# Performance work log

Hardware: AMD Instinct MI355X
Metric: run time of the kernel (lower is better)

The kernel has to match this reference:

```python
import jax, jax.numpy as jnp
import numpy as np

B, D, H = 2048, 64, 512  # batch, state dim, vf hidden dim
IS_DIFFUSION = True      # vf output divided by 2.0 as in CNF.forward


def setup_inputs() -> dict:
    key = jax.random.key(0)
    ks = jax.random.split(key, 8)

    def lin(k, fi, fo):
        return jax.random.normal(k, (fi, fo), jnp.float32) / np.float32(np.sqrt(fi))

    return {
        "t": jax.random.uniform(ks[0], (1,), jnp.float32),      # scalar time, kept as [1]
        "x": jax.random.normal(ks[1], (B, D + 1), jnp.float32),  # last col = logp channel
        "W1": lin(ks[2], D + 1, H),
        "b1": jax.random.normal(ks[3], (H,), jnp.float32) * 0.01,
        "W2": lin(ks[4], H, H),
        "b2": jax.random.normal(ks[5], (H,), jnp.float32) * 0.01,
        "W3": lin(ks[6], H, D),
        "b3": jax.random.normal(ks[7], (D,), jnp.float32) * 0.01,
    }


def reference(t, x, W1, b1, W2, b2, W3, b3):
    scale = 2.0 if IS_DIFFUSION else 1.0
    xd = x[..., :-1]  # [B, D] -- drop augmented log-density channel

    def vf_single(xi):  # R^D -> R^D vector field, t and params closed over
        h = jnp.concatenate([xi, t])           # [D+1] (time-conditioned input)
        h = jnp.tanh(h @ W1 + b1)
        h = jnp.tanh(h @ W2 + b2)
        return (h @ W3 + b3) / scale

    dx = jax.vmap(vf_single)(xd)  # [B, D]
    # exact divergence: trace of per-sample Jacobian via reverse-mode (matches torch jacrev)
    div = jax.vmap(lambda xi: jnp.trace(jax.jacrev(vf_single)(xi)))(xd)  # [B]
    return jnp.concatenate([dx, div[:, None]], axis=-1)  # [B, D+1]
```

## Files before the change

### kernel.cpp

```cpp
#include <hip/hip_runtime.h>


constexpr int HD = 512;
constexpr int DD = 64;
constexpr int SB = 8;
constexpr int NB = 2048 / SB;

typedef __attribute__((ext_vector_type(8))) short bf16x8;
typedef __attribute__((ext_vector_type(4))) float f32x4;

__device__ inline unsigned short f2bf(float f) {
    union { float f; unsigned u; } v; v.f = f;
    return (unsigned short)((v.u + 0x7fffu + ((v.u >> 16) & 1u)) >> 16);
}
__device__ inline float fast_tanh(float xx) {
    float e = __expf(2.f * xx);
    return 1.f - 2.f / (e + 1.f);
}

__global__ __launch_bounds__(64) void cnf_pack_kernel(
    const float* __restrict__ W1, const float* __restrict__ W2,
    const float* __restrict__ W3, unsigned short* __restrict__ Bpack)
{
    __shared__ float w1s[64][33];
    __shared__ float w3s[16][65];
    const int b = blockIdx.x;
    const int mat = b >> 9, t = (b >> 4) & 31, kk = b & 15;
    const int l = threadIdx.x;
    const int q = l >> 4, nl = l & 15;
    const int n = t * 16 + nl;
    unsigned short o[8];
    if (mat == 0) {
#pragma unroll
        for (int j = 0; j < 8; ++j) {
            int k = kk * 32 + q * 8 + j;
            o[j] = f2bf(W2[k * HD + n]);
        }
    } else {
        for (int e = l; e < 64 * 32; e += 64) {
            int i = e >> 5, kl = e & 31;
            w1s[i][kl] = W1[i * HD + kk * 32 + kl];
        }
        for (int e = l; e < 16 * 64; e += 64) {
            int nn = e >> 6, i = e & 63;
            w3s[nn][i] = W3[(t * 16 + nn) * DD + i];
        }
        __syncthreads();
#pragma unroll
        for (int j = 0; j < 8; ++j) {
            int kl = q * 8 + j;
            float m = 0.f;
#pragma unroll 8
            for (int i = 0; i < 64; ++i) m += w1s[i][kl] * w3s[nl][i];
            o[j] = f2bf(W2[(kk * 32 + kl) * HD + n] * m);
        }
    }
    uint4 pk;
    pk.x = (unsigned)o[0] | ((unsigned)o[1] << 16);
    pk.y = (unsigned)o[2] | ((unsigned)o[3] << 16);
    pk.z = (unsigned)o[4] | ((unsigned)o[5] << 16);
    pk.w = (unsigned)o[6] | ((unsigned)o[7] << 16);
    const int w = t >> 2;
    const int t8 = mat * 4 + (t & 3);
    reinterpret_cast<uint4*>(Bpack)[((w * 16 + kk) * 8 + t8) * 64 + l] = pk;
}

__global__ __launch_bounds__(512, 2) void cnf_fused_kernel(
    const float* __restrict__ tptr, const float* __restrict__ x,
    const float* __restrict__ W1, const float* __restrict__ b1,
    const float* __restrict__ b2v, const float* __restrict__ W3,
    const float* __restrict__ b3, const unsigned short* __restrict__ Bpack,
    float* __restrict__ out)
{
    __shared__ float4 xsv[65 * 2];
    __shared__ unsigned short A_lds[16][520];
    __shared__ float4 h2v[HD * 2];
    __shared__ float4 divred[8][2];
    __shared__ float sm_b2[HD];

    const int tid  = threadIdx.x;
    const int s0   = blockIdx.x * SB;
    const int wave = tid >> 6, lane = tid & 63;

    const bf16x8* bp = reinterpret_cast<const bf16x8*>(Bpack)
                     + (size_t)wave * 8192 + lane;
    bf16x8 buf[3][8];
#pragma unroll
    for (int j = 0; j < 8; ++j) buf[0][j] = bp[j * 64];
#pragma unroll
    for (int j = 0; j < 8; ++j) buf[1][j] = bp[512 + j * 64];

    {
        const float tval = tptr[0];
        for (int e = tid; e < SB * 65; e += 512) {
            int s = e / 65, i = e % 65;
            reinterpret_cast<float*>(xsv)[i * SB + s] =
                (i == DD) ? tval : x[(s0 + s) * 65 + i];
        }
        sm_b2[tid] = b2v[tid];
    }
    __syncthreads();

    {
        const int u = tid;
        const float bb = b1[u];
        float2 a0 = {bb, bb}, a1 = {bb, bb}, a2 = {bb, bb}, a3 = {bb, bb};
        for (int ib = 0; ib < 64; ib += 16) {
            float w[16];
#pragma unroll
            for (int qq = 0; qq < 16; ++qq) w[qq] = W1[(ib + qq) * HD + u];
#pragma unroll
            for (int qq = 0; qq < 16; ++qq) {
                float4 p = xsv[2 * (ib + qq)], r = xsv[2 * (ib + qq) + 1];
                a0.x += p.x * w[qq]; a0.y += p.y * w[qq];
                a1.x += p.z * w[qq]; a1.y += p.w * w[qq];
                a2.x += r.x * w[qq]; a2.y += r.y * w[qq];
                a3.x += r.z * w[qq]; a3.y += r.w * w[qq];
            }
        }
        {
            float w = W1[64 * HD + u];
            float4 p = xsv[128], r = xsv[129];
            a0.x += p.x * w; a0.y += p.y * w;
            a1.x += p.z * w; a1.y += p.w * w;
            a2.x += r.x * w; a2.y += r.y * w;
            a3.x += r.z * w; a3.y += r.w * w;
        }
        float h[8] = {fast_tanh(a0.x), fast_tanh(a0.y), fast_tanh(a1.x), fast_tanh(a1.y),
                      fast_tanh(a2.x), fast_tanh(a2.y), fast_tanh(a3.x), fast_tanh(a3.y)};
#pragma unroll
        for (int s = 0; s < 8; ++s) {
            A_lds[s][u]     = f2bf(h[s]);
            A_lds[8 + s][u] = f2bf(1.f - h[s] * h[s]);
        }
    }
    __syncthreads();

    f32x4 cw[4], cg[4];
#pragma unroll
    for (int i = 0; i < 4; ++i) { cw[i] = (f32x4){0,0,0,0}; cg[i] = (f32x4){0,0,0,0}; }
    {
        const unsigned short* arow = &A_lds[lane & 15][0];
        const int aoff = (lane >> 4) * 8;
#pragma unroll
        for (int kk = 0; kk < 16; ++kk) {
            if (kk + 2 < 16) {
#pragma unroll
                for (int j = 0; j < 8; ++j)
                    buf[(kk + 2) % 3][j] = bp[(kk + 2) * 512 + j * 64];
            }
            bf16x8 af = *reinterpret_cast<const bf16x8*>(arow + kk * 32 + aoff);
#pragma unroll
            for (int i = 0; i < 4; ++i)
                cw[i] = __builtin_amdgcn_mfma_f32_16x16x32_bf16(af, buf[kk % 3][i], cw[i], 0, 0, 0);
#pragma unroll
            for (int i = 0; i < 4; ++i)
                cg[i] = __builtin_amdgcn_mfma_f32_16x16x32_bf16(af, buf[kk % 3][4 + i], cg[i], 0, 0, 0);
        }
    }

    {
        const int qd = lane >> 4;
        const int src = (lane >= 32) ? lane - 32 : lane;
        float4 dp = {0.f, 0.f, 0.f, 0.f};
#pragma unroll
        for (int i = 0; i < 4; ++i) {
            const int m = wave * 64 + i * 16 + (lane & 15);
            const float bb = sm_b2[m];
            float4 hv;
            hv.x = fast_tanh(cw[i][0] + bb);
            hv.y = fast_tanh(cw[i][1] + bb);
            hv.z = fast_tanh(cw[i][2] + bb);
            hv.w = fast_tanh(cw[i][3] + bb);
            if (lane < 32) h2v[2 * m + qd] = hv;
            float h0 = __shfl(hv.x, src), h1s = __shfl(hv.y, src);
            float h2s = __shfl(hv.z, src), h3s = __shfl(hv.w, src);
            dp.x += cg[i][0] * (1.f - h0 * h0);
            dp.y += cg[i][1] * (1.f - h1s * h1s);
            dp.z += cg[i][2] * (1.f - h2s * h2s);
            dp.w += cg[i][3] * (1.f - h3s * h3s);
        }
        if (lane >= 32) {
#pragma unroll
            for (int off = 8; off > 0; off >>= 1) {
                dp.x += __shfl_down(dp.x, off, 16);
                dp.y += __shfl_down(dp.y, off, 16);
                dp.z += __shfl_down(dp.z, off, 16);
                dp.w += __shfl_down(dp.w, off, 16);
            }
            if ((lane & 15) == 0) divred[wave][qd - 2] = dp;
        }
    }
    __syncthreads();

    float* opart = reinterpret_cast<float*>(A_lds);

    {
        const int k = lane, part = wave;
        float o[8];
#pragma unroll
        for (int q = 0; q < 8; ++q) o[q] = 0.f;
        const int mb = part * 64;
        for (int mm = 0; mm < 64; mm += 8) {
            float w[8];
#pragma unroll
            for (int q = 0; q < 8; ++q) w[q] = W3[(mb + mm + q) * DD + k];
#pragma unroll
            for (int q = 0; q < 8; ++q) {
                const int m = mb + mm + q;
                float4 ha = h2v[2 * m], hb = h2v[2 * m + 1];
                o[0] += ha.x * w[q]; o[1] += ha.y * w[q];
                o[2] += ha.z * w[q]; o[3] += ha.w * w[q];
                o[4] += hb.x * w[q]; o[5] += hb.y * w[q];
                o[6] += hb.z * w[q]; o[7] += hb.w * w[q];
            }
        }
#pragma unroll
        for (int q = 0; q < 8; ++q) opart[part * 512 + q * 64 + k] = o[q];
    }
    __syncthreads();

    {
        const int s = tid >> 6, k = tid & 63;
        float sum = b3[k];
#pragma unroll
        for (int p = 0; p < 8; ++p) sum += opart[p * 512 + s * 64 + k];
        out[(s0 + s) * 65 + k] = 0.5f * sum;
    }
    if (tid < 8) {
        const int qq = tid >> 2, r = tid & 3;
        float ds = 0.f;
#pragma unroll
        for (int w = 0; w < 8; ++w)
            ds += reinterpret_cast<const float*>(&divred[w][qq])[r];
        out[(s0 + tid) * 65 + DD] = 0.5f * ds;
    }
}

extern "C" void kernel_launch(void* const* d_in, const int* in_sizes, int n_in,
                              void* d_out, int out_size, void* d_ws, size_t ws_size,
                              hipStream_t stream) {
    const float* t  = (const float*)d_in[0];
    const float* x  = (const float*)d_in[1];
    const float* W1 = (const float*)d_in[2];
    const float* b1 = (const float*)d_in[3];
    const float* W2 = (const float*)d_in[4];
    const float* b2 = (const float*)d_in[5];
    const float* W3 = (const float*)d_in[6];
    const float* b3 = (const float*)d_in[7];
    float* out = (float*)d_out;
    unsigned short* Bpack = (unsigned short*)d_ws;

    cnf_pack_kernel<<<1024, 64, 0, stream>>>(W1, W2, W3, Bpack);
    cnf_fused_kernel<<<NB, 512, 0, stream>>>(t, x, W1, b1, b2, W3, b3, Bpack, out);
}
```

Measured before the change: 99.41 us.

## Merge weight packing into main kernel via cooperative launch and grid sync

Folds the separate bf16 weight-packing kernel into the fused kernel. Waves 0-3 of each block pack one slice of W2 or W2*(W1·W3), while waves 4-7 compute the first layer, and a grid-wide cooperative sync follows before the MFMA stage. This removes one kernel launch and overlaps packing with layer-1 compute. In exchange it adds a grid barrier, requires all 256 blocks to be co-resident, and raises shared memory use through a union buffer.

```diff
diff --git a/kernel.cpp b/kernel.cpp
--- a/kernel.cpp
+++ b/kernel.cpp
@@ -1,4 +1,7 @@
 #include <hip/hip_runtime.h>
+#include <hip/hip_cooperative_groups.h>
+
+namespace cg = cooperative_groups;
 
 
 constexpr int HD = 512;
@@ -18,77 +21,33 @@
     return 1.f - 2.f / (e + 1.f);
 }
 
-__global__ __launch_bounds__(64) void cnf_pack_kernel(
-    const float* __restrict__ W1, const float* __restrict__ W2,
-    const float* __restrict__ W3, unsigned short* __restrict__ Bpack)
-{
-    __shared__ float w1s[64][33];
-    __shared__ float w3s[16][65];
-    const int b = blockIdx.x;
-    const int mat = b >> 9, t = (b >> 4) & 31, kk = b & 15;
-    const int l = threadIdx.x;
-    const int q = l >> 4, nl = l & 15;
-    const int n = t * 16 + nl;
-    unsigned short o[8];
-    if (mat == 0) {
-#pragma unroll
-        for (int j = 0; j < 8; ++j) {
-            int k = kk * 32 + q * 8 + j;
-            o[j] = f2bf(W2[k * HD + n]);
-        }
-    } else {
-        for (int e = l; e < 64 * 32; e += 64) {
-            int i = e >> 5, kl = e & 31;
-            w1s[i][kl] = W1[i * HD + kk * 32 + kl];
-        }
-        for (int e = l; e < 16 * 64; e += 64) {
-            int nn = e >> 6, i = e & 63;
-            w3s[nn][i] = W3[(t * 16 + nn) * DD + i];
-        }
-        __syncthreads();
-#pragma unroll
-        for (int j = 0; j < 8; ++j) {
-            int kl = q * 8 + j;
-            float m = 0.f;
-#pragma unroll 8
-            for (int i = 0; i < 64; ++i) m += w1s[i][kl] * w3s[nl][i];
-            o[j] = f2bf(W2[(kk * 32 + kl) * HD + n] * m);
-        }
-    }
-    uint4 pk;
-    pk.x = (unsigned)o[0] | ((unsigned)o[1] << 16);
-    pk.y = (unsigned)o[2] | ((unsigned)o[3] << 16);
-    pk.z = (unsigned)o[4] | ((unsigned)o[5] << 16);
-    pk.w = (unsigned)o[6] | ((unsigned)o[7] << 16);
-    const int w = t >> 2;
-    const int t8 = mat * 4 + (t & 3);
-    reinterpret_cast<uint4*>(Bpack)[((w * 16 + kk) * 8 + t8) * 64 + l] = pk;
-}
-
-__global__ __launch_bounds__(512, 2) void cnf_fused_kernel(
+union SmemBig {
+    struct {
+        float w1s[64 * 132];
+        float w3s[16 * 65];
+    } pk;
+    float4 h2v[HD * 2];
+};
+
+__global__ __launch_bounds__(512, 2) void cnf_mega_kernel(
     const float* __restrict__ tptr, const float* __restrict__ x,
     const float* __restrict__ W1, const float* __restrict__ b1,
-    const float* __restrict__ b2v, const float* __restrict__ W3,
-    const float* __restrict__ b3, const unsigned short* __restrict__ Bpack,
-    float* __restrict__ out)
+    const float* __restrict__ W2, const float* __restrict__ b2v,
+    const float* __restrict__ W3, const float* __restrict__ b3,
+    unsigned short* __restrict__ Bpack, float* __restrict__ out)
 {
+    __shared__ SmemBig sm;
     __shared__ float4 xsv[65 * 2];
     __shared__ unsigned short A_lds[16][520];
-    __shared__ float4 h2v[HD * 2];
+    __shared__ float sm_b2[HD];
     __shared__ float4 divred[8][2];
-    __shared__ float sm_b2[HD];
 
     const int tid  = threadIdx.x;
-    const int s0   = blockIdx.x * SB;
+    const int blk  = blockIdx.x;
+    const int s0   = blk * SB;
     const int wave = tid >> 6, lane = tid & 63;
 
-    const bf16x8* bp = reinterpret_cast<const bf16x8*>(Bpack)
-                     + (size_t)wave * 8192 + lane;
-    bf16x8 buf[3][8];
-#pragma unroll
-    for (int j = 0; j < 8; ++j) buf[0][j] = bp[j * 64];
-#pragma unroll
-    for (int j = 0; j < 8; ++j) buf[1][j] = bp[512 + j * 64];
+    const int mat = blk & 1, t = (blk >> 1) & 31, kkg = blk >> 6;
 
     {
         const float tval = tptr[0];
@@ -98,50 +57,104 @@
                 (i == DD) ? tval : x[(s0 + s) * 65 + i];
         }
         sm_b2[tid] = b2v[tid];
-    }
-    __syncthreads();
-
-    {
-        const int u = tid;
-        const float bb = b1[u];
-        float2 a0 = {bb, bb}, a1 = {bb, bb}, a2 = {bb, bb}, a3 = {bb, bb};
-        for (int ib = 0; ib < 64; ib += 16) {
-            float w[16];
-#pragma unroll
-            for (int qq = 0; qq < 16; ++qq) w[qq] = W1[(ib + qq) * HD + u];
-#pragma unroll
-            for (int qq = 0; qq < 16; ++qq) {
-                float4 p = xsv[2 * (ib + qq)], r = xsv[2 * (ib + qq) + 1];
-                a0.x += p.x * w[qq]; a0.y += p.y * w[qq];
-                a1.x += p.z * w[qq]; a1.y += p.w * w[qq];
-                a2.x += r.x * w[qq]; a2.y += r.y * w[qq];
-                a3.x += r.z * w[qq]; a3.y += r.w * w[qq];
-            }
-        }
-        {
-            float w = W1[64 * HD + u];
-            float4 p = xsv[128], r = xsv[129];
-            a0.x += p.x * w; a0.y += p.y * w;
-            a1.x += p.z * w; a1.y += p.w * w;
-            a2.x += r.x * w; a2.y += r.y * w;
-            a3.x += r.z * w; a3.y += r.w * w;
-        }
-        float h[8] = {fast_tanh(a0.x), fast_tanh(a0.y), fast_tanh(a1.x), fast_tanh(a1.y),
-                      fast_tanh(a2.x), fast_tanh(a2.y), fast_tanh(a3.x), fast_tanh(a3.y)};
-#pragma unroll
-        for (int s = 0; s < 8; ++s) {
-            A_lds[s][u]     = f2bf(h[s]);
-            A_lds[8 + s][u] = f2bf(1.f - h[s] * h[s]);
-        }
-    }
-    __syncthreads();
-
-    f32x4 cw[4], cg[4];
-#pragma unroll
-    for (int i = 0; i < 4; ++i) { cw[i] = (f32x4){0,0,0,0}; cg[i] = (f32x4){0,0,0,0}; }
-    {
+        if (mat) {
+            for (int e = tid; e < 64 * 128; e += 512) {
+                int i = e >> 7, kl = e & 127;
+                sm.pk.w1s[i * 132 + kl] = W1[i * HD + kkg * 128 + kl];
+            }
+            for (int e = tid; e < 16 * 64; e += 512) {
+                int nn = e >> 6, i = e & 63;
+                sm.pk.w3s[nn * 65 + i] = W3[(t * 16 + nn) * DD + i];
+            }
+        }
+    }
+    __syncthreads();
+
+    if (wave < 4) {
+        const int kk = kkg * 4 + wave;
+        const int q = lane >> 4, nl = lane & 15;
+        const int n = t * 16 + nl;
+        unsigned short o[8];
+        if (mat == 0) {
+#pragma unroll
+            for (int j = 0; j < 8; ++j)
+                o[j] = f2bf(W2[(kk * 32 + q * 8 + j) * HD + n]);
+        } else {
+            float s[8];
+#pragma unroll
+            for (int j = 0; j < 8; ++j) s[j] = 0.f;
+            const int kl0 = wave * 32 + q * 8;
+#pragma unroll 4
+            for (int i = 0; i < 64; ++i) {
+                const float w3v = sm.pk.w3s[nl * 65 + i];
+#pragma unroll
+                for (int j = 0; j < 8; ++j)
+                    s[j] += sm.pk.w1s[i * 132 + kl0 + j] * w3v;
+            }
+#pragma unroll
+            for (int j = 0; j < 8; ++j)
+                o[j] = f2bf(W2[(kk * 32 + q * 8 + j) * HD + n] * s[j]);
+        }
+        uint4 pk4;
+        pk4.x = (unsigned)o[0] | ((unsigned)o[1] << 16);
+        pk4.y = (unsigned)o[2] | ((unsigned)o[3] << 16);
+        pk4.z = (unsigned)o[4] | ((unsigned)o[5] << 16);
+        pk4.w = (unsigned)o[6] | ((unsigned)o[7] << 16);
+        const int w = t >> 2, t8 = mat * 4 + (t & 3);
+        reinterpret_cast<uint4*>(Bpack)[((w * 16 + kk) * 8 + t8) * 64 + lane] = pk4;
+    } else {
+        const int u0 = tid - 256;
+#pragma unroll
+        for (int hu = 0; hu < 2; ++hu) {
+            const int u = u0 + hu * 256;
+            const float bb = b1[u];
+            float2 a0 = {bb, bb}, a1 = {bb, bb}, a2 = {bb, bb}, a3 = {bb, bb};
+            for (int ib = 0; ib < 64; ib += 8) {
+                float w[8];
+#pragma unroll
+                for (int qq = 0; qq < 8; ++qq) w[qq] = W1[(ib + qq) * HD + u];
+#pragma unroll
+                for (int qq = 0; qq < 8; ++qq) {
+                    float4 p = xsv[2 * (ib + qq)], r = xsv[2 * (ib + qq) + 1];
+                    a0.x += p.x * w[qq]; a0.y += p.y * w[qq];
+                    a1.x += p.z * w[qq]; a1.y += p.w * w[qq];
+                    a2.x += r.x * w[qq]; a2.y += r.y * w[qq];
+                    a3.x += r.z * w[qq]; a3.y += r.w * w[qq];
+                }
+            }
+            {
+                float w = W1[64 * HD + u];
+                float4 p = xsv[128], r = xsv[129];
+                a0.x += p.x * w; a0.y += p.y * w;
+                a1.x += p.z * w; a1.y += p.w * w;
+                a2.x += r.x * w; a2.y += r.y * w;
+                a3.x += r.z * w; a3.y += r.w * w;
+            }
+            float h[8] = {fast_tanh(a0.x), fast_tanh(a0.y), fast_tanh(a1.x), fast_tanh(a1.y),
+                          fast_tanh(a2.x), fast_tanh(a2.y), fast_tanh(a3.x), fast_tanh(a3.y)};
+#pragma unroll
+            for (int s = 0; s < 8; ++s) {
+                A_lds[s][u]     = f2bf(h[s]);
+                A_lds[8 + s][u] = f2bf(1.f - h[s] * h[s]);
+            }
+        }
+    }
+    __syncthreads();
+    cg::this_grid().sync();
+
+    f32x4 cw[4], cg4[4];
+#pragma unroll
+    for (int i = 0; i < 4; ++i) { cw[i] = (f32x4){0,0,0,0}; cg4[i] = (f32x4){0,0,0,0}; }
+    {
+        const bf16x8* bp = reinterpret_cast<const bf16x8*>(Bpack)
+                         + (size_t)wave * 8192 + lane;
         const unsigned short* arow = &A_lds[lane & 15][0];
         const int aoff = (lane >> 4) * 8;
+        bf16x8 buf[3][8];
+#pragma unroll
+        for (int j = 0; j < 8; ++j) buf[0][j] = bp[j * 64];
+#pragma unroll
+        for (int j = 0; j < 8; ++j) buf[1][j] = bp[512 + j * 64];
 #pragma unroll
         for (int kk = 0; kk < 16; ++kk) {
             if (kk + 2 < 16) {
@@ -155,7 +168,7 @@
                 cw[i] = __builtin_amdgcn_mfma_f32_16x16x32_bf16(af, buf[kk % 3][i], cw[i], 0, 0, 0);
 #pragma unroll
             for (int i = 0; i < 4; ++i)
-                cg[i] = __builtin_amdgcn_mfma_f32_16x16x32_bf16(af, buf[kk % 3][4 + i], cg[i], 0, 0, 0);
+                cg4[i] = __builtin_amdgcn_mfma_f32_16x16x32_bf16(af, buf[kk % 3][4 + i], cg4[i], 0, 0, 0);
         }
     }
 
@@ -172,13 +185,13 @@
             hv.y = fast_tanh(cw[i][1] + bb);
             hv.z = fast_tanh(cw[i][2] + bb);
             hv.w = fast_tanh(cw[i][3] + bb);
-            if (lane < 32) h2v[2 * m + qd] = hv;
+            if (lane < 32) sm.h2v[2 * m + qd] = hv;
             float h0 = __shfl(hv.x, src), h1s = __shfl(hv.y, src);
             float h2s = __shfl(hv.z, src), h3s = __shfl(hv.w, src);
-            dp.x += cg[i][0] * (1.f - h0 * h0);
-            dp.y += cg[i][1] * (1.f - h1s * h1s);
-            dp.z += cg[i][2] * (1.f - h2s * h2s);
-            dp.w += cg[i][3] * (1.f - h3s * h3s);
+            dp.x += cg4[i][0] * (1.f - h0 * h0);
+            dp.y += cg4[i][1] * (1.f - h1s * h1s);
+            dp.z += cg4[i][2] * (1.f - h2s * h2s);
+            dp.w += cg4[i][3] * (1.f - h3s * h3s);
         }
         if (lane >= 32) {
 #pragma unroll
@@ -208,7 +221,7 @@
 #pragma unroll
             for (int q = 0; q < 8; ++q) {
                 const int m = mb + mm + q;
-                float4 ha = h2v[2 * m], hb = h2v[2 * m + 1];
+                float4 ha = sm.h2v[2 * m], hb = sm.h2v[2 * m + 1];
                 o[0] += ha.x * w[q]; o[1] += ha.y * w[q];
                 o[2] += ha.z * w[q]; o[3] += ha.w * w[q];
                 o[4] += hb.x * w[q]; o[5] += hb.y * w[q];
@@ -251,6 +264,9 @@
     float* out = (float*)d_out;
     unsigned short* Bpack = (unsigned short*)d_ws;
 
-    cnf_pack_kernel<<<1024, 64, 0, stream>>>(W1, W2, W3, Bpack);
-    cnf_fused_kernel<<<NB, 512, 0, stream>>>(t, x, W1, b1, b2, W3, b3, Bpack, out);
-}
+    void* args[10] = { (void*)&t, (void*)&x, (void*)&W1, (void*)&b1,
+                       (void*)&W2, (void*)&b2, (void*)&W3, (void*)&b3,
+                       (void*)&Bpack, (void*)&out };
+    hipLaunchCooperativeKernel((const void*)cnf_mega_kernel,
+                               dim3(NB), dim3(512), args, 0, stream);
+}
```

Result: slower. 126.9 us (+27.6%).
